# Optimization experiments

Measured on AMD Instinct MI355X. Metric: run time of the kernel, lower is better.

The kernel has to match this reference:

```python
import jax, jax.numpy as jnp
import numpy as np

B, S, D, H = 4, 2048, 1024, 16
DK = D // H


def setup_inputs() -> dict:
    key = jax.random.key(0)
    ks = jax.random.split(key, 5)
    scale = 1.0 / np.sqrt(D)
    return {
        "embeddings": jax.random.normal(ks[0], (B, S, D), dtype=jnp.float32),
        "W_q": jax.random.normal(ks[1], (D, D), dtype=jnp.float32) * scale,
        "W_k": jax.random.normal(ks[2], (D, D), dtype=jnp.float32) * scale,
        "W_v": jax.random.normal(ks[3], (D, D), dtype=jnp.float32) * scale,
        "W_o": jax.random.normal(ks[4], (D, D), dtype=jnp.float32) * scale,
    }


def reference(embeddings, W_q, W_k, W_v, W_o):
    # torch Linear: y = x @ W.T  (weights stored [out, in])
    def proj(x, W):
        # [B,S,D] -> [B,H,S,DK]
        y = jnp.einsum("bsd,ed->bse", x, W)
        return y.reshape(B, S, H, DK).transpose(0, 2, 1, 3)

    Q = proj(embeddings, W_q)
    K = proj(embeddings, W_k)
    V = proj(embeddings, W_v)

    scores = jnp.einsum("bhqd,bhkd->bhqk", Q, K) / jnp.sqrt(jnp.float32(DK))
    p_attn = jax.nn.softmax(scores, axis=-1)  # dropout p=0.0 -> identity
    x = jnp.einsum("bhqk,bhkd->bhqd", p_attn, V)
    x = x.transpose(0, 2, 1, 3).reshape(B, S, D)
    return jnp.einsum("bsd,ed->bse", x, W_o)
```

## Files before the change

### kernel.cpp

```cpp
#include <hip/hip_runtime.h>
#include <hip/hip_bf16.h>

#define BB 4
#define SS 2048
#define DD 1024
#define HH 16
#define MM (BB * SS)

typedef __attribute__((ext_vector_type(8))) short bf16x8;
typedef __attribute__((ext_vector_type(4))) float f32x4;

__device__ __forceinline__ unsigned short f2bf(float f) {
  union { float f; unsigned u; } v; v.f = f;
  unsigned r = v.u + 0x7fffu + ((v.u >> 16) & 1u);
  return (unsigned short)(r >> 16);
}

__device__ __forceinline__ void gl2lds16(const void* g, void* l) {
  __builtin_amdgcn_global_load_lds(
      (const __attribute__((address_space(1))) unsigned int*)g,
      (__attribute__((address_space(3))) unsigned int*)l, 16, 0, 0);
}

__global__ __launch_bounds__(256)
void convall(const float* __restrict__ X, const float* __restrict__ a,
             const float* __restrict__ b, const float* __restrict__ c,
             const float* __restrict__ d, unsigned short* __restrict__ wall,
             unsigned short* __restrict__ xb) {
  int y = blockIdx.y;
  const float* s; unsigned short* o;
  if (y < 4) {
    const float* srcs[4] = {a, b, c, d};
    s = srcs[y]; o = wall + (size_t)y * 1048576;
  } else {
    s = X + (size_t)(y - 4) * 1048576; o = xb + (size_t)(y - 4) * 1048576;
  }
  int i = (blockIdx.x * 256 + threadIdx.x) * 4;
  float4 v = *(const float4*)(s + i);
  ushort4 h4; h4.x = f2bf(v.x); h4.y = f2bf(v.y); h4.z = f2bf(v.z); h4.w = f2bf(v.w);
  *(ushort4*)(o + i) = h4;
}

template<int OMODE>
__global__ __launch_bounds__(256)
void gemm_k(const unsigned short* __restrict__ A16, const unsigned short* __restrict__ Bp,
            void* __restrict__ C0p, void* __restrict__ C1p, void* __restrict__ C2p) {
  __shared__ unsigned short As[32 * 136];
  __shared__ unsigned short Bs[128 * 32];
  const int m0 = blockIdx.x * 128, n0g = blockIdx.y * 128;
  const int tid = threadIdx.x, lane = tid & 63, wave = tid >> 6;
  const int wm = (wave & 1) * 64, wn = (wave >> 1) * 64;
  const int row_in = lane & 15, quad = lane >> 4;

  f32x4 acc[4][4] = {};

  for (int kb = 0; kb < DD; kb += 32) {
    {
      int r = wave * 32 + (lane >> 2);
      const unsigned short* g = Bp + (size_t)(n0g + r) * DD + kb + (lane & 3) * 8;
      gl2lds16(g, Bs + (wave * 32) * 32);
      gl2lds16(g + (size_t)16 * DD, Bs + (wave * 32 + 16) * 32);
      const unsigned short* ga = A16 + (size_t)(m0 + r) * DD + kb + (lane & 3) * 8;
      gl2lds16(ga, As + (wave * 32) * 32);
      gl2lds16(ga + (size_t)16 * DD, As + (wave * 32 + 16) * 32);
    }
    __syncthreads();
    bf16x8 af[4], bfr[4];
#pragma unroll
    for (int i = 0; i < 4; ++i)
      af[i] = *(const bf16x8*)(As + (wm + i * 16 + row_in) * 32 + quad * 8);
#pragma unroll
    for (int j = 0; j < 4; ++j)
      bfr[j] = *(const bf16x8*)(Bs + (wn + j * 16 + row_in) * 32 + quad * 8);
#pragma unroll
    for (int i = 0; i < 4; ++i)
#pragma unroll
      for (int j = 0; j < 4; ++j)
        acc[i][j] = __builtin_amdgcn_mfma_f32_16x16x32_bf16(af[i], bfr[j], acc[i][j], 0, 0, 0);
    __syncthreads();
  }

  if (OMODE == 1) {
    float* Cout = (float*)C0p;
#pragma unroll
    for (int i = 0; i < 4; ++i)
#pragma unroll
      for (int j = 0; j < 4; ++j)
#pragma unroll
        for (int r = 0; r < 4; ++r)
          Cout[(size_t)(m0 + wm + i * 16 + quad * 4 + r) * DD + n0g + wn + j * 16 + row_in] =
              acc[i][j][r];
  } else {
    const int seg = n0g >> 10;
    if (seg < 2) {
      unsigned short* Cout = (unsigned short*)(seg == 0 ? C0p : C1p);
      const int n0 = n0g & 1023;
#pragma unroll
      for (int i = 0; i < 4; ++i)
#pragma unroll
        for (int j = 0; j < 4; ++j)
#pragma unroll
          for (int r = 0; r < 4; ++r)
            Cout[(size_t)(m0 + wm + i * 16 + quad * 4 + r) * DD + n0 + wn + j * 16 + row_in] =
                f2bf(acc[i][j][r]);
    } else {
      unsigned short* Vt = (unsigned short*)C2p;
      unsigned short* Ts = As;
      const int b = m0 >> 11, m_in_b = m0 & 2047;
      const int nv = n0g - 2048;
#pragma unroll
      for (int cn = 0; cn < 4; ++cn) {
        if ((wave >> 1) == (cn >> 1)) {
#pragma unroll
          for (int i = 0; i < 4; ++i)
#pragma unroll
            for (int jj = 0; jj < 2; ++jj)
#pragma unroll
              for (int r = 0; r < 4; ++r) {
                int j = (cn & 1) * 2 + jj;
                Ts[(jj * 16 + row_in) * 136 + wm + i * 16 + quad * 4 + r] = f2bf(acc[i][j][r]);
              }
        }
        __syncthreads();
#pragma unroll
        for (int it = 0; it < 2; ++it) {
          int cc = tid + it * 256;
          int rowL = cc >> 4, o8 = (cc & 15) * 8;
          int cbase = rowL * 136 + (o8 & 64) + ((o8 & 63) >> 2);
          ushort4 lo, hi;
          lo.x = Ts[cbase];      lo.y = Ts[cbase + 16];
          lo.z = Ts[cbase + 32]; lo.w = Ts[cbase + 48];
          hi.x = Ts[cbase + 1];  hi.y = Ts[cbase + 17];
          hi.z = Ts[cbase + 33]; hi.w = Ts[cbase + 49];
          int n = nv + cn * 32 + rowL;
          int h = n >> 6, dd = n & 63;
          unsigned short* dst = Vt + ((size_t)((b * 16 + h) * 64 + dd)) * SS + m_in_b + o8;
          *(ushort4*)dst = lo;
          *(ushort4*)(dst + 4) = hi;
        }
        __syncthreads();
      }
    }
  }
}

__global__ __launch_bounds__(256, 4)
void attn_kernel(const unsigned short* __restrict__ Q, const unsigned short* __restrict__ K,
                 const unsigned short* __restrict__ Vt_g, unsigned short* __restrict__ AO) {
  __shared__ unsigned short Ks[64 * 72];
  __shared__ unsigned short Vs[64 * 72];
  __shared__ unsigned short Ps[128 * 72];
  const int L = (blockIdx.y << 4) + blockIdx.x;
  const int jj = L >> 3;
  const int qt = jj & 15;
  const int bh = (L & 7) + ((jj >> 4) << 3);
  const int b = bh >> 4, h = bh & 15;
  const int tid = threadIdx.x, lane = tid & 63, w = tid >> 6;
  const int row_in = lane & 15, quad = lane >> 4;
  const float Cs = 0.180336880f;
  const float C0 = 17.3123405f;
  const size_t qbase = ((size_t)(b * SS + qt * 128)) * DD + h * 64;

  bf16x8 aq[2][2];
#pragma unroll
  for (int m = 0; m < 2; ++m) {
    const unsigned short* qp = Q + qbase + (size_t)(w * 32 + m * 16 + row_in) * DD;
    aq[m][0] = *(const bf16x8*)(qp + quad * 8);
    aq[m][1] = *(const bf16x8*)(qp + 32 + quad * 8);
  }
  f32x4 oacc[2][4] = {};
  float lrow[2][4] = {};
  const int permr = 2 * (row_in >> 2) + (row_in & 1) + 8 * ((row_in >> 1) & 1);
  const int pw_base = (w * 32) * 72;

  const int r0 = tid >> 3, o80 = (tid & 7) * 8;
  const int r1 = (tid + 256) >> 3, o81 = o80;
  const unsigned short* kp0 = K + ((size_t)(b * SS + r0)) * DD + h * 64 + o80;
  const unsigned short* kp1 = K + ((size_t)(b * SS + r1)) * DD + h * 64 + o81;
  const unsigned short* vp0 = Vt_g + ((size_t)(bh * 64 + r0)) * SS + o80;
  const unsigned short* vp1 = Vt_g + ((size_t)(bh * 64 + r1)) * SS + o81;

  uint4 kr0 = *(const uint4*)kp0;
  uint4 kr1 = *(const uint4*)kp1;
  uint4 vr0 = *(const uint4*)vp0;
  uint4 vr1 = *(const uint4*)vp1;

  for (int kt = 0; kt < SS / 64; ++kt) {
    __syncthreads();
    *(uint4*)(Ks + r0 * 72 + o80) = kr0;
    *(uint4*)(Ks + r1 * 72 + o81) = kr1;
    *(uint4*)(Vs + r0 * 72 + o80) = vr0;
    *(uint4*)(Vs + r1 * 72 + o81) = vr1;
    __syncthreads();
    if (kt + 1 < SS / 64) {
      const size_t ko = (size_t)(kt + 1) * 64 * DD;
      const size_t vo = (size_t)(kt + 1) * 64;
      kr0 = *(const uint4*)(kp0 + ko);
      kr1 = *(const uint4*)(kp1 + ko);
      vr0 = *(const uint4*)(vp0 + vo);
      vr1 = *(const uint4*)(vp1 + vo);
    }

    f32x4 sacc[2][4] = {};
    __builtin_amdgcn_s_setprio(1);
#pragma unroll
    for (int n = 0; n < 4; ++n) {
      bf16x8 bk0 = *(const bf16x8*)(Ks + (n * 16 + row_in) * 72 + quad * 8);
      bf16x8 bk1 = *(const bf16x8*)(Ks + (n * 16 + row_in) * 72 + 32 + quad * 8);
#pragma unroll
      for (int m = 0; m < 2; ++m) {
        sacc[m][n] = __builtin_amdgcn_mfma_f32_16x16x32_bf16(aq[m][0], bk0, sacc[m][n], 0, 0, 0);
        sacc[m][n] = __builtin_amdgcn_mfma_f32_16x16x32_bf16(aq[m][1], bk1, sacc[m][n], 0, 0, 0);
      }
    }
    __builtin_amdgcn_s_setprio(0);

#pragma unroll
    for (int m = 0; m < 2; ++m)
#pragma unroll
      for (int r = 0; r < 4; ++r) {
        int prow = pw_base + (m * 16 + 2 * quad + (r & 1) + 8 * ((r >> 1) & 1)) * 72;
        union { float f; unsigned u; } p0, p1, p2, p3;
        p0.f = __builtin_amdgcn_exp2f(fmaf(sacc[m][0][r], Cs, -C0));
        p1.f = __builtin_amdgcn_exp2f(fmaf(sacc[m][1][r], Cs, -C0));
        p2.f = __builtin_amdgcn_exp2f(fmaf(sacc[m][2][r], Cs, -C0));
        p3.f = __builtin_amdgcn_exp2f(fmaf(sacc[m][3][r], Cs, -C0));
        lrow[m][r] += (p0.f + p1.f) + (p2.f + p3.f);
        unsigned w01 = __builtin_amdgcn_perm(p1.u + 0x8000u, p0.u + 0x8000u, 0x07060302);
        unsigned w23 = __builtin_amdgcn_perm(p3.u + 0x8000u, p2.u + 0x8000u, 0x07060302);
        *(uint2*)(Ps + prow + row_in * 4) = make_uint2(w01, w23);
      }

    __builtin_amdgcn_s_setprio(1);
#pragma unroll
    for (int c = 0; c < 2; ++c) {
      bf16x8 ap0 = *(const bf16x8*)(Ps + pw_base + (permr) * 72 + c * 32 + quad * 8);
      bf16x8 ap1 = *(const bf16x8*)(Ps + pw_base + (16 + permr) * 72 + c * 32 + quad * 8);
#pragma unroll
      for (int t = 0; t < 4; ++t) {
        bf16x8 bv = *(const bf16x8*)(Vs + (t * 16 + row_in) * 72 + c * 32 + quad * 8);
        oacc[0][t] = __builtin_amdgcn_mfma_f32_16x16x32_bf16(ap0, bv, oacc[0][t], 0, 0, 0);
        oacc[1][t] = __builtin_amdgcn_mfma_f32_16x16x32_bf16(ap1, bv, oacc[1][t], 0, 0, 0);
      }
    }
    __builtin_amdgcn_s_setprio(0);
  }

#pragma unroll
  for (int m = 0; m < 2; ++m)
#pragma unroll
    for (int r = 0; r < 4; ++r) {
#pragma unroll
      for (int s = 1; s < 16; s <<= 1) lrow[m][r] += __shfl_xor(lrow[m][r], s, 64);
      float inv = 1.0f / lrow[m][r];
#pragma unroll
      for (int t = 0; t < 4; ++t)
        AO[qbase + (size_t)(w * 32 + m * 16 + quad * 4 + r) * DD + t * 16 + row_in] =
            f2bf(oacc[m][t][r] * inv);
    }
}

extern "C" void kernel_launch(void* const* d_in, const int* in_sizes, int n_in,
                              void* d_out, int out_size, void* d_ws, size_t ws_size,
                              hipStream_t stream) {
  const float* X  = (const float*)d_in[0];
  const float* Wq = (const float*)d_in[1];
  const float* Wk = (const float*)d_in[2];
  const float* Wv = (const float*)d_in[3];
  const float* Wo = (const float*)d_in[4];

  unsigned short* ws   = (unsigned short*)d_ws;
  unsigned short* Qb   = ws;
  unsigned short* Kb   = Qb + (size_t)MM * DD;
  unsigned short* Vtb  = Kb + (size_t)MM * DD;
  unsigned short* Wall = Vtb + (size_t)MM * DD;
  unsigned short* Xb   = (unsigned short*)d_out;
  float* out = (float*)d_out;

  convall<<<dim3(1024, 12), 256, 0, stream>>>(X, Wq, Wk, Wv, Wo, Wall, Xb);

  gemm_k<3><<<dim3(MM / 128, 24), 256, 0, stream>>>(Xb, Wall, Qb, Kb, Vtb);

  attn_kernel<<<dim3(SS / 128, BB * HH), 256, 0, stream>>>(Qb, Kb, Vtb, Qb);

  gemm_k<1><<<dim3(MM / 128, 8), 256, 0, stream>>>(Qb, Wall + (size_t)3 * 1048576,
                                                   out, nullptr, nullptr);
}
```

Baseline: 269.1 us.

## Double attention query tile to 256 rows per block for K/V reuse

Each attention block now handles 256 query rows (64 per wave) instead of 128, so every K/V tile loaded into LDS feeds twice as many MFMAs, and grid size is halved. K fragments are hoisted into registers and the score/softmax step runs per 16-row sub-tile to limit live accumulators. The cost is more registers and a doubled P buffer in LDS, which lowers occupancy (launch bounds drop from 4 to 2 blocks) and leaves fewer blocks to spread across CUs.

After: 270.4 us. Within noise of the previous version (+0.5%).

```diff
diff --git a/kernel.cpp b/kernel.cpp
--- a/kernel.cpp
+++ b/kernel.cpp
@@ -144,34 +144,33 @@
   }
 }
 
-__global__ __launch_bounds__(256, 4)
+__global__ __launch_bounds__(256, 2)
 void attn_kernel(const unsigned short* __restrict__ Q, const unsigned short* __restrict__ K,
                  const unsigned short* __restrict__ Vt_g, unsigned short* __restrict__ AO) {
   __shared__ unsigned short Ks[64 * 72];
   __shared__ unsigned short Vs[64 * 72];
-  __shared__ unsigned short Ps[128 * 72];
-  const int L = (blockIdx.y << 4) + blockIdx.x;
-  const int jj = L >> 3;
-  const int qt = jj & 15;
-  const int bh = (L & 7) + ((jj >> 4) << 3);
+  __shared__ unsigned short Ps[256 * 72];
+  const int L = (blockIdx.y << 3) + blockIdx.x;
+  const int qt = (L >> 3) & 7;
+  const int bh = (L & 7) + ((L >> 6) << 3);
   const int b = bh >> 4, h = bh & 15;
   const int tid = threadIdx.x, lane = tid & 63, w = tid >> 6;
   const int row_in = lane & 15, quad = lane >> 4;
   const float Cs = 0.180336880f;
   const float C0 = 17.3123405f;
-  const size_t qbase = ((size_t)(b * SS + qt * 128)) * DD + h * 64;
-
-  bf16x8 aq[2][2];
-#pragma unroll
-  for (int m = 0; m < 2; ++m) {
-    const unsigned short* qp = Q + qbase + (size_t)(w * 32 + m * 16 + row_in) * DD;
+  const size_t qbase = ((size_t)(b * SS + qt * 256)) * DD + h * 64;
+
+  bf16x8 aq[4][2];
+#pragma unroll
+  for (int m = 0; m < 4; ++m) {
+    const unsigned short* qp = Q + qbase + (size_t)(w * 64 + m * 16 + row_in) * DD;
     aq[m][0] = *(const bf16x8*)(qp + quad * 8);
     aq[m][1] = *(const bf16x8*)(qp + 32 + quad * 8);
   }
-  f32x4 oacc[2][4] = {};
-  float lrow[2][4] = {};
+  f32x4 oacc[4][4] = {};
+  float lrow[4][4] = {};
   const int permr = 2 * (row_in >> 2) + (row_in & 1) + 8 * ((row_in >> 1) & 1);
-  const int pw_base = (w * 32) * 72;
+  const int pw_base = (w * 64) * 72;
 
   const int r0 = tid >> 3, o80 = (tid & 7) * 8;
   const int r1 = (tid + 256) >> 3, o81 = o80;
@@ -201,53 +200,59 @@
       vr1 = *(const uint4*)(vp1 + vo);
     }
 
-    f32x4 sacc[2][4] = {};
-    __builtin_amdgcn_s_setprio(1);
+    bf16x8 bk[4][2];
 #pragma unroll
     for (int n = 0; n < 4; ++n) {
-      bf16x8 bk0 = *(const bf16x8*)(Ks + (n * 16 + row_in) * 72 + quad * 8);
-      bf16x8 bk1 = *(const bf16x8*)(Ks + (n * 16 + row_in) * 72 + 32 + quad * 8);
-#pragma unroll
-      for (int m = 0; m < 2; ++m) {
-        sacc[m][n] = __builtin_amdgcn_mfma_f32_16x16x32_bf16(aq[m][0], bk0, sacc[m][n], 0, 0, 0);
-        sacc[m][n] = __builtin_amdgcn_mfma_f32_16x16x32_bf16(aq[m][1], bk1, sacc[m][n], 0, 0, 0);
-      }
-    }
-    __builtin_amdgcn_s_setprio(0);
-
-#pragma unroll
-    for (int m = 0; m < 2; ++m)
+      bk[n][0] = *(const bf16x8*)(Ks + (n * 16 + row_in) * 72 + quad * 8);
+      bk[n][1] = *(const bf16x8*)(Ks + (n * 16 + row_in) * 72 + 32 + quad * 8);
+    }
+
+#pragma unroll
+    for (int m = 0; m < 4; ++m) {
+      f32x4 sacc[4] = {};
+      __builtin_amdgcn_s_setprio(1);
+#pragma unroll
+      for (int n = 0; n < 4; ++n) {
+        sacc[n] = __builtin_amdgcn_mfma_f32_16x16x32_bf16(aq[m][0], bk[n][0], sacc[n], 0, 0, 0);
+        sacc[n] = __builtin_amdgcn_mfma_f32_16x16x32_bf16(aq[m][1], bk[n][1], sacc[n], 0, 0, 0);
+      }
+      __builtin_amdgcn_s_setprio(0);
+
 #pragma unroll
       for (int r = 0; r < 4; ++r) {
         int prow = pw_base + (m * 16 + 2 * quad + (r & 1) + 8 * ((r >> 1) & 1)) * 72;
         union { float f; unsigned u; } p0, p1, p2, p3;
-        p0.f = __builtin_amdgcn_exp2f(fmaf(sacc[m][0][r], Cs, -C0));
-        p1.f = __builtin_amdgcn_exp2f(fmaf(sacc[m][1][r], Cs, -C0));
-        p2.f = __builtin_amdgcn_exp2f(fmaf(sacc[m][2][r], Cs, -C0));
-        p3.f = __builtin_amdgcn_exp2f(fmaf(sacc[m][3][r], Cs, -C0));
+        p0.f = __builtin_amdgcn_exp2f(fmaf(sacc[0][r], Cs, -C0));
+        p1.f = __builtin_amdgcn_exp2f(fmaf(sacc[1][r], Cs, -C0));
+        p2.f = __builtin_amdgcn_exp2f(fmaf(sacc[2][r], Cs, -C0));
+        p3.f = __builtin_amdgcn_exp2f(fmaf(sacc[3][r], Cs, -C0));
         lrow[m][r] += (p0.f + p1.f) + (p2.f + p3.f);
         unsigned w01 = __builtin_amdgcn_perm(p1.u + 0x8000u, p0.u + 0x8000u, 0x07060302);
         unsigned w23 = __builtin_amdgcn_perm(p3.u + 0x8000u, p2.u + 0x8000u, 0x07060302);
         *(uint2*)(Ps + prow + row_in * 4) = make_uint2(w01, w23);
       }
+    }
 
     __builtin_amdgcn_s_setprio(1);
 #pragma unroll
     for (int c = 0; c < 2; ++c) {
-      bf16x8 ap0 = *(const bf16x8*)(Ps + pw_base + (permr) * 72 + c * 32 + quad * 8);
-      bf16x8 ap1 = *(const bf16x8*)(Ps + pw_base + (16 + permr) * 72 + c * 32 + quad * 8);
+      bf16x8 ap[4];
+#pragma unroll
+      for (int mm = 0; mm < 4; ++mm)
+        ap[mm] = *(const bf16x8*)(Ps + pw_base + (mm * 16 + permr) * 72 + c * 32 + quad * 8);
 #pragma unroll
       for (int t = 0; t < 4; ++t) {
         bf16x8 bv = *(const bf16x8*)(Vs + (t * 16 + row_in) * 72 + c * 32 + quad * 8);
-        oacc[0][t] = __builtin_amdgcn_mfma_f32_16x16x32_bf16(ap0, bv, oacc[0][t], 0, 0, 0);
-        oacc[1][t] = __builtin_amdgcn_mfma_f32_16x16x32_bf16(ap1, bv, oacc[1][t], 0, 0, 0);
+#pragma unroll
+        for (int mm = 0; mm < 4; ++mm)
+          oacc[mm][t] = __builtin_amdgcn_mfma_f32_16x16x32_bf16(ap[mm], bv, oacc[mm][t], 0, 0, 0);
       }
     }
     __builtin_amdgcn_s_setprio(0);
   }
 
 #pragma unroll
-  for (int m = 0; m < 2; ++m)
+  for (int m = 0; m < 4; ++m)
 #pragma unroll
     for (int r = 0; r < 4; ++r) {
 #pragma unroll
@@ -255,7 +260,7 @@
       float inv = 1.0f / lrow[m][r];
 #pragma unroll
       for (int t = 0; t < 4; ++t)
-        AO[qbase + (size_t)(w * 32 + m * 16 + quad * 4 + r) * DD + t * 16 + row_in] =
+        AO[qbase + (size_t)(w * 64 + m * 16 + quad * 4 + r) * DD + t * 16 + row_in] =
             f2bf(oacc[m][t][r] * inv);
     }
 }
@@ -281,7 +286,7 @@
 
   gemm_k<3><<<dim3(MM / 128, 24), 256, 0, stream>>>(Xb, Wall, Qb, Kb, Vtb);
 
-  attn_kernel<<<dim3(SS / 128, BB * HH), 256, 0, stream>>>(Qb, Kb, Vtb, Qb);
+  attn_kernel<<<dim3(SS / 256, BB * HH), 256, 0, stream>>>(Qb, Kb, Vtb, Qb);
 
   gemm_k<1><<<dim3(MM / 128, 8), 256, 0, stream>>>(Qb, Wall + (size_t)3 * 1048576,
                                                    out, nullptr, nullptr);
```
